# Optimization experiments

Hardware: AMD Instinct MI355X
Metric: run time of the kernel (lower is better)

Reference implementation:

```python
import jax, jax.numpy as jnp
import numpy as np

N = 2048      # layer_size
R = 4         # displacement rank
B = 4096      # batch
STD = 0.01    # init_stddev


def toeplitz_mult(G, H, x):
    """out[b] = sum_i Krylov(Z_1, g_i) @ Krylov(Z_{-1}, h_i)^T @ x[b]   (cycle=True, f=(1,-1)).

    Krylov(Z_1, g) is the circulant matrix C(g) with first column g:
        C(g)[i, j] = g[(i-j) mod n]
    Krylov(Z_{-1}, h) is the skew-circulant S(h):
        S(h)[i, j] = h[(i-j) mod n] * (-1 if i < j else 1)
    Using the factorization S(h) = D^{-1} C(D h) D with D = diag(eta^k), eta = exp(i*pi/n):
        S(h)^T x = D C((D h)') D^{-1} x,   where c'[k] = c[(-k) mod n]
    and circulant products are done via FFT: C(c) u = ifft(fft(c) * fft(u)).
    """
    r, n = G.shape
    eta = jnp.exp(1j * jnp.pi * jnp.arange(n) / n).astype(jnp.complex64)  # (n,)
    # ---- transpose Krylov multiply with f = -1:  U_i = S(h_i)^T x,  shape (r, b, n) ----
    Hm = H.astype(jnp.complex64) * eta                      # D h_i, (r, n)
    Hm_rev = jnp.roll(Hm[:, ::-1], 1, axis=-1)              # c'[k] = c[(-k) mod n]
    xm = x.astype(jnp.complex64) / eta                      # D^{-1} x, (b, n)
    U = jnp.fft.ifft(jnp.fft.fft(Hm_rev)[:, None, :] * jnp.fft.fft(xm)[None, :, :], axis=-1)
    U = (U * eta).real                                      # S(h_i)^T x is real, (r, b, n)
    # ---- Krylov multiply with f = 1:  Y_i = C(g_i) U_i ----
    Gf = jnp.fft.fft(G.astype(jnp.complex64))[:, None, :]   # (r, 1, n)
    Y = jnp.fft.ifft(Gf * jnp.fft.fft(U.astype(jnp.complex64), axis=-1), axis=-1).real
    return Y.sum(0)                                         # (b, n)


def setup_inputs() -> dict:
    key = jax.random.key(0)
    k1, k2, k3 = jax.random.split(key, 3)
    x = jax.random.normal(k1, (B, N), jnp.float32)
    G = jax.random.normal(k2, (R, N), jnp.float32) * STD
    H = jax.random.normal(k3, (R, N), jnp.float32) * STD
    return {"x": x, "G": G, "H": H}


def reference(x, G, H):
    return toeplitz_mult(G, H, x)
```

## Files before the change

kernel.cpp:

```cpp
#include <hip/hip_runtime.h>
#include <cstdint>
#include <cstddef>

constexpr int kN = 2048;
constexpr int kB = 4096;
constexpr int kR = 4;

typedef __attribute__((ext_vector_type(4))) float f32x4;
typedef __attribute__((ext_vector_type(8))) short short8;
typedef __attribute__((ext_vector_type(8))) unsigned short ushort8;

__device__ __forceinline__ unsigned short f2bf(float f) {
  unsigned u = __float_as_uint(f);
  u += 0x7FFFu + ((u >> 16) & 1u);
  return (unsigned short)(u >> 16);
}

__device__ __forceinline__ void gload_lds16(const void* g, void* l) {
  __builtin_amdgcn_global_load_lds(
      (const __attribute__((address_space(1))) void*)g,
      (__attribute__((address_space(3))) void*)l, 16, 0, 0);
}

__global__ void prep_kernel(const float* __restrict__ x,
                            const float* __restrict__ G,
                            const float* __restrict__ H,
                            unsigned short* __restrict__ xb,
                            unsigned short* __restrict__ Dp) {
  __shared__ float wsum[4];
  const int tid = threadIdx.x;

  if (blockIdx.x < (kB * kN) / (256 * 8)) {
    const int t = blockIdx.x * 256 + tid;
    const float4* xv = (const float4*)x;
    float4 a = xv[t * 2];
    float4 b = xv[t * 2 + 1];
    ushort8 o;
    o[0] = f2bf(a.x); o[1] = f2bf(a.y); o[2] = f2bf(a.z); o[3] = f2bf(a.w);
    o[4] = f2bf(b.x); o[5] = f2bf(b.y); o[6] = f2bf(b.z); o[7] = f2bf(b.w);
    *(ushort8*)(xb + (size_t)t * 8) = o;
    return;
  }

  const int d = blockIdx.x - (kB * kN) / (256 * 8);
  const int lane = tid & 63, wave = tid >> 6;
  const int v0 = tid * 8;

  float loc[8];
  float run = 0.f;
#pragma unroll
  for (int jj = 0; jj < 8; ++jj) {
    const int v = v0 + jj;
    float q = 0.f;
#pragma unroll
    for (int t = 0; t < kR; ++t)
      q += G[t * kN + ((v + d) & (kN - 1))] * H[t * kN + v];
    run += q;
    loc[jj] = run;
  }

  float incl = run;
#pragma unroll
  for (int off = 1; off < 64; off <<= 1) {
    float tv = __shfl_up(incl, off, 64);
    if (lane >= off) incl += tv;
  }
  if (lane == 63) wsum[wave] = incl;
  __syncthreads();
  float woff = 0.f, total = 0.f;
#pragma unroll
  for (int w = 0; w < 4; ++w) {
    const float s = wsum[w];
    total += s;
    if (w < wave) woff += s;
  }
  const float exc = woff + incl - run;

  ushort8 o;
#pragma unroll
  for (int jj = 0; jj < 8; ++jj)
    o[jj] = f2bf(2.f * (exc + loc[jj]) - total);
  *(ushort8*)(Dp + (size_t)d * kN + v0) = o;
}

__global__ void build_M_kernel(const unsigned short* __restrict__ Dp,
                               unsigned short* __restrict__ Mb) {
  __shared__ unsigned short lds[128][64];
  const int tid = threadIdx.x;
  const int i0 = blockIdx.y * 64, j0 = blockIdx.x * 64;
  const int delta0 = (i0 - j0 - 63) & (kN - 1);
#pragma unroll
  for (int it = 0; it < 32; ++it) {
    const int lin = it * 256 + tid;
    const int dd = lin >> 6, jj = lin & 63;
    lds[dd][jj] = Dp[(size_t)((delta0 + dd) & (kN - 1)) * kN + j0 + jj];
  }
  __syncthreads();
#pragma unroll
  for (int it = 0; it < 16; ++it) {
    const int lin = it * 256 + tid;
    const int ii = lin >> 6, jj = lin & 63;
    Mb[(size_t)(i0 + ii) * kN + j0 + jj] = lds[ii - jj + 63][jj];
  }
}

__global__ __launch_bounds__(256) void gemm_kernel(
    const unsigned short* __restrict__ A,
    const unsigned short* __restrict__ Bt,
    float* __restrict__ C) {
  __shared__ unsigned short As[2][8192];
  __shared__ unsigned short Bs[2][8192];

  const int tid = threadIdx.x;
  const int lane = tid & 63, wave = tid >> 6;
  const int wr = wave >> 1, wc = wave & 1;
  const int r16 = lane & 15, kg = lane >> 4;

  const int flat = blockIdx.y * gridDim.x + blockIdx.x;
  const int swz = (flat & 7) * 64 + (flat >> 3);
  const int by = swz >> 4, bx = swz & 15;
  const int row0 = by * 128, col0 = bx * 128;

  const unsigned short* Abase = A + (size_t)row0 * kN;
  const unsigned short* Bbase = Bt + (size_t)col0 * kN;
  const int ldsw = wave * 1024;

  f32x4 acc[4][4] = {};

  auto stage = [&](const unsigned short* src, unsigned short* dstbase) {
#pragma unroll
    for (int i = 0; i < 4; ++i) {
      const int r = (i & 1) * 64 + (tid >> 2);
      const int gbyte = r * (kN * 2) + (i >> 1) * 64
                        + (((tid & 3) ^ (r & 3)) * 16);
      gload_lds16((const char*)src + gbyte, (char*)dstbase + i * 4096 + ldsw);
    }
  };

  stage(Abase, As[0]);
  stage(Bbase, Bs[0]);
  __syncthreads();

  for (int t = 0; t < kN / 64; ++t) {
    const int cur = t & 1;
    if (t < kN / 64 - 1) {
      stage(Abase + (t + 1) * 64, As[cur ^ 1]);
      stage(Bbase + (t + 1) * 64, Bs[cur ^ 1]);
    }
    __builtin_amdgcn_sched_barrier(0);

    short8 af[2][4], bf[2][4];
#pragma unroll
    for (int s = 0; s < 2; ++s)
#pragma unroll
      for (int mt = 0; mt < 4; ++mt) {
        const int row = wr * 64 + mt * 16 + r16;
        af[s][mt] = *(const short8*)&As[cur][s * 4096 + row * 32 + ((kg ^ (row & 3)) << 3)];
      }
#pragma unroll
    for (int s = 0; s < 2; ++s)
#pragma unroll
      for (int nt = 0; nt < 4; ++nt) {
        const int row = wc * 64 + nt * 16 + r16;
        bf[s][nt] = *(const short8*)&Bs[cur][s * 4096 + row * 32 + ((kg ^ (row & 3)) << 3)];
      }
#pragma unroll
    for (int mt = 0; mt < 4; ++mt)
#pragma unroll
      for (int nt = 0; nt < 4; ++nt)
#pragma unroll
        for (int s = 0; s < 2; ++s)
          acc[mt][nt] = __builtin_amdgcn_mfma_f32_16x16x32_bf16(
              af[s][mt], bf[s][nt], acc[mt][nt], 0, 0, 0);

    __syncthreads();
  }

#pragma unroll
  for (int mt = 0; mt < 4; ++mt)
#pragma unroll
    for (int nt = 0; nt < 4; ++nt) {
      const int r = row0 + wr * 64 + mt * 16 + kg * 4;
      const int c = col0 + wc * 64 + nt * 16 + r16;
#pragma unroll
      for (int j = 0; j < 4; ++j)
        C[(size_t)(r + j) * kN + c] = acc[mt][nt][j];
    }
}

extern "C" void kernel_launch(void* const* d_in, const int* in_sizes, int n_in,
                              void* d_out, int out_size, void* d_ws, size_t ws_size,
                              hipStream_t stream) {
  const float* x = (const float*)d_in[0];
  const float* G = (const float*)d_in[1];
  const float* H = (const float*)d_in[2];
  float* out = (float*)d_out;

  char* ws = (char*)d_ws;
  unsigned short* Mb = (unsigned short*)ws;
  unsigned short* xb = (unsigned short*)(ws + (8u << 20));
  unsigned short* Dp = (unsigned short*)(ws + (24u << 20));

  const int cast_blocks = (kB * kN) / (256 * 8);
  prep_kernel<<<dim3(cast_blocks + kN), dim3(256), 0, stream>>>(x, G, H, xb, Dp);
  build_M_kernel<<<dim3(kN / 64, kN / 64), dim3(256), 0, stream>>>(Dp, Mb);
  gemm_kernel<<<dim3(kN / 128, kB / 128), dim3(256), 0, stream>>>(xb, Mb, out);
}
```

Baseline: 165.9 us.

## Triple-buffer GEMM with 256x128 tiles, 512 threads and interleaved load/MFMA phases

Reworks the bf16 GEMM kernel so each block computes a 256x128 tile with 8 waves. Shared memory becomes a 3-stage ring, and tile t+2 is prefetched while tile t is computed. Explicit vmcnt waits, barriers and setprio interleave the global-to-LDS loads with the MFMA phases. The LDS swizzle widens to 8 chunks to avoid bank conflicts. The goal is to hide memory latency and raise B-tile reuse, at the cost of more LDS per block (lower occupancy) and fragile hand-written wait counts.

```diff
diff --git a/kernel.cpp b/kernel.cpp
--- a/kernel.cpp
+++ b/kernel.cpp
@@ -104,12 +104,12 @@
   }
 }
 
-__global__ __launch_bounds__(256) void gemm_kernel(
+__global__ __launch_bounds__(512, 1) void gemm_kernel(
     const unsigned short* __restrict__ A,
     const unsigned short* __restrict__ Bt,
     float* __restrict__ C) {
-  __shared__ unsigned short As[2][8192];
-  __shared__ unsigned short Bs[2][8192];
+  __shared__ unsigned short As[3][256 * 64];
+  __shared__ unsigned short Bs[3][128 * 64];
 
   const int tid = threadIdx.x;
   const int lane = tid & 63, wave = tid >> 6;
@@ -117,63 +117,89 @@
   const int r16 = lane & 15, kg = lane >> 4;
 
   const int flat = blockIdx.y * gridDim.x + blockIdx.x;
-  const int swz = (flat & 7) * 64 + (flat >> 3);
+  const int swz = (flat & 7) * 32 + (flat >> 3);
   const int by = swz >> 4, bx = swz & 15;
-  const int row0 = by * 128, col0 = bx * 128;
-
-  const unsigned short* Abase = A + (size_t)row0 * kN;
-  const unsigned short* Bbase = Bt + (size_t)col0 * kN;
-  const int ldsw = wave * 1024;
+  const int row0 = by * 256, col0 = bx * 128;
+
+  const char* Abase = (const char*)(A + (size_t)row0 * kN);
+  const char* Bbase = (const char*)(Bt + (size_t)col0 * kN);
+
+  int aoff[4], boff[2];
+#pragma unroll
+  for (int i = 0; i < 4; ++i) {
+    const int slot = i * 512 + tid;
+    const int r = slot >> 3, cl = slot & 7;
+    aoff[i] = r * (kN * 2) + ((cl ^ (r & 7)) << 4);
+  }
+#pragma unroll
+  for (int i = 0; i < 2; ++i) {
+    const int slot = i * 512 + tid;
+    const int r = slot >> 3, cl = slot & 7;
+    boff[i] = r * (kN * 2) + ((cl ^ (r & 7)) << 4);
+  }
 
   f32x4 acc[4][4] = {};
 
-  auto stage = [&](const unsigned short* src, unsigned short* dstbase) {
-#pragma unroll
-    for (int i = 0; i < 4; ++i) {
-      const int r = (i & 1) * 64 + (tid >> 2);
-      const int gbyte = r * (kN * 2) + (i >> 1) * 64
-                        + (((tid & 3) ^ (r & 3)) * 16);
-      gload_lds16((const char*)src + gbyte, (char*)dstbase + i * 4096 + ldsw);
+#define STAGE_A(kt, buf, i) \
+  gload_lds16(Abase + aoff[i] + (kt) * 128, (char*)As[buf] + ((i) * 512 + tid) * 16)
+#define STAGE_B(kt, buf, i) \
+  gload_lds16(Bbase + boff[i] + (kt) * 128, (char*)Bs[buf] + ((i) * 512 + tid) * 16)
+
+#pragma unroll
+  for (int i = 0; i < 4; ++i) STAGE_A(0, 0, i);
+#pragma unroll
+  for (int i = 0; i < 2; ++i) STAGE_B(0, 0, i);
+#pragma unroll
+  for (int i = 0; i < 4; ++i) STAGE_A(1, 1, i);
+#pragma unroll
+  for (int i = 0; i < 2; ++i) STAGE_B(1, 1, i);
+
+  for (int t = 0; t < kN / 64; ++t) {
+    const int cur = t % 3, nxt = (t + 2) % 3;
+    const bool more = (t + 2) < kN / 64;
+
+    if (t < kN / 64 - 1) asm volatile("s_waitcnt vmcnt(6)" ::: "memory");
+    else                 asm volatile("s_waitcnt vmcnt(0)" ::: "memory");
+    __builtin_amdgcn_s_barrier();
+
+    const char* abuf = (const char*)As[cur];
+    const char* bbuf = (const char*)Bs[cur];
+
+    short8 bfr[4][2];
+#pragma unroll
+    for (int nt = 0; nt < 4; ++nt) {
+      const int brow = wc * 64 + nt * 16 + r16;
+#pragma unroll
+      for (int s = 0; s < 2; ++s)
+        bfr[nt][s] = *(const short8*)(bbuf + brow * 128 + (((s * 4 + kg) ^ (brow & 7)) << 4));
     }
-  };
-
-  stage(Abase, As[0]);
-  stage(Bbase, Bs[0]);
-  __syncthreads();
-
-  for (int t = 0; t < kN / 64; ++t) {
-    const int cur = t & 1;
-    if (t < kN / 64 - 1) {
-      stage(Abase + (t + 1) * 64, As[cur ^ 1]);
-      stage(Bbase + (t + 1) * 64, Bs[cur ^ 1]);
+
+#define PHASE(mt, STAGES)                                                       \
+    {                                                                           \
+      const int arow = wr * 64 + (mt) * 16 + r16;                               \
+      short8 af0 = *(const short8*)(abuf + arow * 128 + (((kg) ^ (arow & 7)) << 4));       \
+      short8 af1 = *(const short8*)(abuf + arow * 128 + (((4 + kg) ^ (arow & 7)) << 4));   \
+      STAGES;                                                                   \
+      __builtin_amdgcn_s_barrier();                                             \
+      asm volatile("s_waitcnt lgkmcnt(0)" ::: "memory");                        \
+      __builtin_amdgcn_sched_barrier(0);                                        \
+      __builtin_amdgcn_s_setprio(1);                                            \
+      acc[mt][0] = __builtin_amdgcn_mfma_f32_16x16x32_bf16(af0, bfr[0][0], acc[mt][0], 0, 0, 0); \
+      acc[mt][0] = __builtin_amdgcn_mfma_f32_16x16x32_bf16(af1, bfr[0][1], acc[mt][0], 0, 0, 0); \
+      acc[mt][1] = __builtin_amdgcn_mfma_f32_16x16x32_bf16(af0, bfr[1][0], acc[mt][1], 0, 0, 0); \
+      acc[mt][1] = __builtin_amdgcn_mfma_f32_16x16x32_bf16(af1, bfr[1][1], acc[mt][1], 0, 0, 0); \
+      acc[mt][2] = __builtin_amdgcn_mfma_f32_16x16x32_bf16(af0, bfr[2][0], acc[mt][2], 0, 0, 0); \
+      acc[mt][2] = __builtin_amdgcn_mfma_f32_16x16x32_bf16(af1, bfr[2][1], acc[mt][2], 0, 0, 0); \
+      acc[mt][3] = __builtin_amdgcn_mfma_f32_16x16x32_bf16(af0, bfr[3][0], acc[mt][3], 0, 0, 0); \
+      acc[mt][3] = __builtin_amdgcn_mfma_f32_16x16x32_bf16(af1, bfr[3][1], acc[mt][3], 0, 0, 0); \
+      __builtin_amdgcn_s_setprio(0);                                            \
     }
-    __builtin_amdgcn_sched_barrier(0);
-
-    short8 af[2][4], bf[2][4];
-#pragma unroll
-    for (int s = 0; s < 2; ++s)
-#pragma unroll
-      for (int mt = 0; mt < 4; ++mt) {
-        const int row = wr * 64 + mt * 16 + r16;
-        af[s][mt] = *(const short8*)&As[cur][s * 4096 + row * 32 + ((kg ^ (row & 3)) << 3)];
-      }
-#pragma unroll
-    for (int s = 0; s < 2; ++s)
-#pragma unroll
-      for (int nt = 0; nt < 4; ++nt) {
-        const int row = wc * 64 + nt * 16 + r16;
-        bf[s][nt] = *(const short8*)&Bs[cur][s * 4096 + row * 32 + ((kg ^ (row & 3)) << 3)];
-      }
-#pragma unroll
-    for (int mt = 0; mt < 4; ++mt)
-#pragma unroll
-      for (int nt = 0; nt < 4; ++nt)
-#pragma unroll
-        for (int s = 0; s < 2; ++s)
-          acc[mt][nt] = __builtin_amdgcn_mfma_f32_16x16x32_bf16(
-              af[s][mt], bf[s][nt], acc[mt][nt], 0, 0, 0);
-
-    __syncthreads();
+
+    PHASE(0, if (more) { STAGE_A(t + 2, nxt, 0); STAGE_A(t + 2, nxt, 1); });
+    PHASE(1, if (more) { STAGE_A(t + 2, nxt, 2); STAGE_A(t + 2, nxt, 3); });
+    PHASE(2, if (more) { STAGE_B(t + 2, nxt, 0); STAGE_B(t + 2, nxt, 1); });
+    PHASE(3, );
+#undef PHASE
   }
 
 #pragma unroll
@@ -204,5 +230,5 @@
   const int cast_blocks = (kB * kN) / (256 * 8);
   prep_kernel<<<dim3(cast_blocks + kN), dim3(256), 0, stream>>>(x, G, H, xb, Dp);
   build_M_kernel<<<dim3(kN / 64, kN / 64), dim3(256), 0, stream>>>(Dp, Mb);
-  gemm_kernel<<<dim3(kN / 128, kB / 128), dim3(256), 0, stream>>>(xb, Mb, out);
-}
+  gemm_kernel<<<dim3(kN / 128, kB / 256), dim3(512), 0, stream>>>(xb, Mb, out);
+}
```

Result: slower. 171.9 us (+3.7%).

## Triple-buffer GEMM K-loop with BK=32, partial vmcnt waits and MFMA priority

Applied to the files above, without the earlier changes.

Restructures the bf16 GEMM main loop from a double-buffered BK=64 pipeline into a triple-buffered BK=32 pipeline. Each iteration waits with a partial s_waitcnt vmcnt and a single barrier, so loads for tile t+2 stay in flight while tile t is computed. LDS use drops, launch bounds request two blocks per CU, and s_setprio raises wave priority around the MFMA block. The cost is twice as many loop iterations and barriers, plus hand-written waitcnt logic that must match the number of outstanding LDS-direct loads.

```diff
diff --git a/kernel.cpp b/kernel.cpp
--- a/kernel.cpp
+++ b/kernel.cpp
@@ -104,12 +104,12 @@
   }
 }
 
-__global__ __launch_bounds__(256) void gemm_kernel(
+__global__ __launch_bounds__(256, 2) void gemm_kernel(
     const unsigned short* __restrict__ A,
     const unsigned short* __restrict__ Bt,
     float* __restrict__ C) {
-  __shared__ unsigned short As[2][8192];
-  __shared__ unsigned short Bs[2][8192];
+  __shared__ unsigned short As[3][128 * 32];
+  __shared__ unsigned short Bs[3][128 * 32];
 
   const int tid = threadIdx.x;
   const int lane = tid & 63, wave = tid >> 6;
@@ -121,60 +121,67 @@
   const int by = swz >> 4, bx = swz & 15;
   const int row0 = by * 128, col0 = bx * 128;
 
-  const unsigned short* Abase = A + (size_t)row0 * kN;
-  const unsigned short* Bbase = Bt + (size_t)col0 * kN;
-  const int ldsw = wave * 1024;
+  const char* Abase = (const char*)(A + (size_t)row0 * kN);
+  const char* Bbase = (const char*)(Bt + (size_t)col0 * kN);
+
+  int goff[2];
+#pragma unroll
+  for (int i = 0; i < 2; ++i) {
+    const int slot = i * 256 + tid;
+    const int r = slot >> 2, cl = slot & 3;
+    goff[i] = r * (kN * 2) + ((cl ^ (r & 3)) << 4);
+  }
 
   f32x4 acc[4][4] = {};
 
-  auto stage = [&](const unsigned short* src, unsigned short* dstbase) {
-#pragma unroll
-    for (int i = 0; i < 4; ++i) {
-      const int r = (i & 1) * 64 + (tid >> 2);
-      const int gbyte = r * (kN * 2) + (i >> 1) * 64
-                        + (((tid & 3) ^ (r & 3)) * 16);
-      gload_lds16((const char*)src + gbyte, (char*)dstbase + i * 4096 + ldsw);
+#define STAGE(kt, buf)                                                        \
+  {                                                                           \
+    _Pragma("unroll")                                                         \
+    for (int i = 0; i < 2; ++i) {                                             \
+      gload_lds16(Abase + goff[i] + (kt) * 64,                                \
+                  (char*)As[buf] + (i * 256 + tid) * 16);                     \
+      gload_lds16(Bbase + goff[i] + (kt) * 64,                                \
+                  (char*)Bs[buf] + (i * 256 + tid) * 16);                     \
+    }                                                                         \
+  }
+
+  STAGE(0, 0);
+  STAGE(1, 1);
+
+  const int NT = kN / 32;
+  for (int t = 0; t < NT; ++t) {
+    const int cur = t % 3, nxt = (t + 2) % 3;
+
+    if (t < NT - 1) asm volatile("s_waitcnt vmcnt(4)" ::: "memory");
+    else            asm volatile("s_waitcnt vmcnt(0)" ::: "memory");
+    __builtin_amdgcn_s_barrier();
+
+    if (t + 2 < NT) STAGE(t + 2, nxt);
+    __builtin_amdgcn_sched_barrier(0);
+
+    const char* abuf = (const char*)As[cur];
+    const char* bbuf = (const char*)Bs[cur];
+    short8 af[4], bf[4];
+#pragma unroll
+    for (int mt = 0; mt < 4; ++mt) {
+      const int row = wr * 64 + mt * 16 + r16;
+      af[mt] = *(const short8*)(abuf + row * 64 + ((kg ^ (row & 3)) << 4));
     }
-  };
-
-  stage(Abase, As[0]);
-  stage(Bbase, Bs[0]);
-  __syncthreads();
-
-  for (int t = 0; t < kN / 64; ++t) {
-    const int cur = t & 1;
-    if (t < kN / 64 - 1) {
-      stage(Abase + (t + 1) * 64, As[cur ^ 1]);
-      stage(Bbase + (t + 1) * 64, Bs[cur ^ 1]);
+#pragma unroll
+    for (int nt = 0; nt < 4; ++nt) {
+      const int row = wc * 64 + nt * 16 + r16;
+      bf[nt] = *(const short8*)(bbuf + row * 64 + ((kg ^ (row & 3)) << 4));
     }
-    __builtin_amdgcn_sched_barrier(0);
-
-    short8 af[2][4], bf[2][4];
-#pragma unroll
-    for (int s = 0; s < 2; ++s)
-#pragma unroll
-      for (int mt = 0; mt < 4; ++mt) {
-        const int row = wr * 64 + mt * 16 + r16;
-        af[s][mt] = *(const short8*)&As[cur][s * 4096 + row * 32 + ((kg ^ (row & 3)) << 3)];
-      }
-#pragma unroll
-    for (int s = 0; s < 2; ++s)
-#pragma unroll
-      for (int nt = 0; nt < 4; ++nt) {
-        const int row = wc * 64 + nt * 16 + r16;
-        bf[s][nt] = *(const short8*)&Bs[cur][s * 4096 + row * 32 + ((kg ^ (row & 3)) << 3)];
-      }
+    __builtin_amdgcn_s_setprio(1);
 #pragma unroll
     for (int mt = 0; mt < 4; ++mt)
 #pragma unroll
       for (int nt = 0; nt < 4; ++nt)
-#pragma unroll
-        for (int s = 0; s < 2; ++s)
-          acc[mt][nt] = __builtin_amdgcn_mfma_f32_16x16x32_bf16(
-              af[s][mt], bf[s][nt], acc[mt][nt], 0, 0, 0);
-
-    __syncthreads();
-  }
+        acc[mt][nt] = __builtin_amdgcn_mfma_f32_16x16x32_bf16(
+            af[mt], bf[nt], acc[mt][nt], 0, 0, 0);
+    __builtin_amdgcn_s_setprio(0);
+  }
+#undef STAGE
 
 #pragma unroll
   for (int mt = 0; mt < 4; ++mt)
```

Result: slower. 171.8 us (+3.6%).
